# Kernel tuning notes

Measured on AMD Instinct MI355X. Metric: run time of the kernel, lower is better.

Reference implementation:

```python
import jax, jax.numpy as jnp
import numpy as np

NEG_SLOPE = 0.2
EPS = 1e-16

N_NODES = 50000
N_EDGES = 800000
IN_C = 256
HID_C = 64
HEADS = 4
OUT_C = 128
N_GRAPHS = 100


def setup_inputs() -> dict:
    key = jax.random.key(0)
    ks = jax.random.split(key, 12)
    x = jax.random.normal(ks[0], (N_NODES, IN_C), dtype=jnp.float32)
    edge_index = jax.random.randint(ks[1], (2, N_EDGES), 0, N_NODES, dtype=jnp.int64)
    batch = jnp.sort(jax.random.randint(ks[2], (N_NODES,), 0, N_GRAPHS, dtype=jnp.int64))
    s1 = 1.0 / np.sqrt(IN_C)
    s2 = 1.0 / np.sqrt(HEADS * HID_C)
    W1 = jax.random.uniform(ks[3], (IN_C, HEADS * HID_C), jnp.float32, -s1, s1)
    att_src1 = jax.random.uniform(ks[4], (HEADS, HID_C), jnp.float32, -s1, s1)
    att_dst1 = jax.random.uniform(ks[5], (HEADS, HID_C), jnp.float32, -s1, s1)
    bias1 = jnp.zeros((HEADS * HID_C,), jnp.float32)
    W2 = jax.random.uniform(ks[6], (HEADS * HID_C, OUT_C), jnp.float32, -s2, s2)
    att_src2 = jax.random.uniform(ks[7], (1, OUT_C), jnp.float32, -s2, s2)
    att_dst2 = jax.random.uniform(ks[8], (1, OUT_C), jnp.float32, -s2, s2)
    bias2 = jnp.zeros((OUT_C,), jnp.float32)
    return {"x": x, "W1": W1, "att_src1": att_src1, "att_dst1": att_dst1,
            "bias1": bias1, "W2": W2, "att_src2": att_src2, "att_dst2": att_dst2,
            "bias2": bias2, "edge_index": edge_index, "batch": batch,
            "num_graphs": N_GRAPHS}


def gat_conv(x, W, att_src, att_dst, bias, src, dst, heads, ch):
    # x: [N, F_in]; W: [F_in, heads*ch]; att_*: [heads, ch]
    n = x.shape[0]
    h = (x @ W).reshape(n, heads, ch)                      # [N, H, C]
    a_src = jnp.sum(h * att_src[None], axis=-1)            # [N, H]
    a_dst = jnp.sum(h * att_dst[None], axis=-1)            # [N, H]
    alpha = a_src[src] + a_dst[dst]                        # [E, H]
    alpha = jax.nn.leaky_relu(alpha, NEG_SLOPE)
    # segment softmax over destination nodes (every node has a self-loop)
    amax = jax.ops.segment_max(alpha, dst, num_segments=n)
    e = jnp.exp(alpha - amax[dst])
    denom = jax.ops.segment_sum(e, dst, num_segments=n)
    alpha = e / (denom[dst] + EPS)                         # [E, H]
    msg = h[src] * alpha[:, :, None]                       # [E, H, C]
    out = jax.ops.segment_sum(msg, dst, num_segments=n)    # [N, H, C]
    return out.reshape(n, heads * ch) + bias


def reference(x, W1, att_src1, att_dst1, bias1, W2, att_src2, att_dst2, bias2,
              edge_index, batch, num_graphs):
    n = x.shape[0]
    loops = jnp.arange(n, dtype=edge_index.dtype)
    src = jnp.concatenate([edge_index[0], loops])
    dst = jnp.concatenate([edge_index[1], loops])
    h = gat_conv(x, W1, att_src1, att_dst1, bias1, src, dst, HEADS, HID_C)
    h = jax.nn.relu(h)
    h = gat_conv(h, W2, att_src2, att_dst2, bias2, src, dst, 1, OUT_C)
    h = jax.nn.relu(h)
    # global mean pool over graphs
    sums = jax.ops.segment_sum(h, batch, num_segments=num_graphs)
    cnt = jax.ops.segment_sum(jnp.ones((n, 1), h.dtype), batch, num_segments=num_graphs)
    return sums / jnp.maximum(cnt, 1.0)
```

## Files before the change

kernel.cpp:

```cpp
#include <hip/hip_runtime.h>
#include <hip/hip_bf16.h>
#include <hip/hip_fp16.h>

#define N_NODES 50000
#define N_EDGES 800000
#define E_TOT   (N_EDGES + N_NODES)
#define IN_C    256
#define H1C     256
#define HEADS   4
#define HID_C   64
#define OUT_C   128
#define N_GRAPHS 100
#define NEG_SLOPE 0.2f
#define EPS_F 1e-16f

#define NBUCKET 391
#define BIN_BLOCKS 104
#define EDGES_PER_SB 8192
#define EBUF_CAP 4096
#define STAGE_CAP 4096
#define GEMM1_MB 391

#define PREP_CAST_BLOCKS   12500
#define PREP_W1_BLOCKS     256
#define PREP_W2_BLOCKS     128
#define PREP_BOUNDS_BLOCKS 196
#define PREP_ZERO_BLOCKS   52
#define PREP_TOTAL (PREP_CAST_BLOCKS + PREP_W1_BLOCKS + PREP_W2_BLOCKS + PREP_BOUNDS_BLOCKS + PREP_ZERO_BLOCKS)

typedef _Float16 half8_t __attribute__((ext_vector_type(8)));
typedef float f32x4 __attribute__((ext_vector_type(4)));

__global__ __launch_bounds__(256) void prep_kernel(const float* __restrict__ x,
                                                   _Float16* __restrict__ xh,
                                                   const float* __restrict__ W1,
                                                   _Float16* __restrict__ W1t,
                                                   const float* __restrict__ W2,
                                                   _Float16* __restrict__ W2t,
                                                   const int* __restrict__ batch,
                                                   int* __restrict__ gstart,
                                                   int* __restrict__ gcur,
                                                   float* __restrict__ d_out) {
    int b = blockIdx.x;
    int tid = threadIdx.x;
    if (b < PREP_CAST_BLOCKS) {
        int idx = b * 256 + tid;
        float4 v = reinterpret_cast<const float4*>(x)[idx];
        union { _Float16 h[4]; uint2 u; } p;
        p.h[0] = (_Float16)v.x; p.h[1] = (_Float16)v.y;
        p.h[2] = (_Float16)v.z; p.h[3] = (_Float16)v.w;
        reinterpret_cast<uint2*>(xh)[idx] = p.u;
        return;
    }
    b -= PREP_CAST_BLOCKS;
    if (b < PREP_W1_BLOCKS) {
        int idx = b * 256 + tid;
        int n = idx >> 8, k = idx & 255;
        W1t[idx] = (_Float16)W1[k * 256 + n];
        return;
    }
    b -= PREP_W1_BLOCKS;
    if (b < PREP_W2_BLOCKS) {
        int idx = b * 256 + tid;
        int n = idx >> 8, k = idx & 255;
        W2t[idx] = (_Float16)W2[k * 128 + n];
        return;
    }
    b -= PREP_W2_BLOCKS;
    if (b < PREP_BOUNDS_BLOCKS) {
        int idx = b * 256 + tid;
        if (idx >= N_NODES) return;
        int g = batch[idx];
        if (g < 0) g = 0; if (g >= N_GRAPHS) g = N_GRAPHS - 1;
        if (idx == 0) {
            for (int j = 0; j <= g; ++j) gstart[j] = 0;
        } else {
            int gp = batch[idx - 1];
            if (gp < 0) gp = 0; if (gp >= N_GRAPHS) gp = N_GRAPHS - 1;
            for (int j = gp + 1; j <= g; ++j) gstart[j] = idx;
        }
        if (idx == N_NODES - 1) {
            for (int j = g + 1; j <= N_GRAPHS; ++j) gstart[j] = N_NODES;
        }
        return;
    }
    b -= PREP_BOUNDS_BLOCKS;
    {
        int idx = b * 256 + tid;
        if (idx < N_GRAPHS * 128) d_out[idx] = 0.f;
        else {
            int k = idx - N_GRAPHS * 128;
            if (k < 512) gcur[k] = 0;
        }
    }
}

__global__ __launch_bounds__(256) void bucket_bin(const int* __restrict__ ei,
                                                  int* __restrict__ gcur,
                                                  int* __restrict__ ebuf) {
    __shared__ int bh[NBUCKET];
    __shared__ int bofs[NBUCKET];
    int tid = threadIdx.x;
    for (int t = tid; t < NBUCKET; t += 256) bh[t] = 0;
    __syncthreads();
    int base = blockIdx.x * EDGES_PER_SB;
#pragma unroll 4
    for (int k = 0; k < EDGES_PER_SB / 256; ++k) {
        int idx = base + k * 256 + tid;
        int d = -1;
        if (idx < N_EDGES) d = ei[N_EDGES + idx];
        else if (idx < E_TOT) d = idx - N_EDGES;
        if (d >= 0 && d < N_NODES) atomicAdd(&bh[d >> 7], 1);
    }
    __syncthreads();
    for (int t = tid; t < NBUCKET; t += 256) {
        int c = bh[t];
        bofs[t] = (c > 0) ? atomicAdd(&gcur[t], c) : 0;
        bh[t] = 0;
    }
    __syncthreads();
#pragma unroll 4
    for (int k = 0; k < EDGES_PER_SB / 256; ++k) {
        int idx = base + k * 256 + tid;
        int s = 0, d = -1;
        if (idx < N_EDGES) { s = ei[idx]; d = ei[N_EDGES + idx]; }
        else if (idx < E_TOT) { s = idx - N_EDGES; d = s; }
        if (d >= 0 && d < N_NODES) {
            int t = d >> 7;
            int p = bofs[t] + atomicAdd(&bh[t], 1);
            if (p < EBUF_CAP)
                ebuf[t * EBUF_CAP + p] = (s & 0xFFFF) | ((d & 127) << 16);
        }
    }
}

__global__ __launch_bounds__(256) void sort_gemm1_kernel(const int* __restrict__ gcur,
                                                         const int* __restrict__ ebuf,
                                                         int* __restrict__ ssrc,
                                                         int* __restrict__ row_ptr,
                                                         const _Float16* __restrict__ A,
                                                         const _Float16* __restrict__ Bt,
                                                         _Float16* __restrict__ C,
                                                         const float* __restrict__ attS,
                                                         const float* __restrict__ attD,
                                                         float* __restrict__ a_src_o,
                                                         float* __restrict__ a_dst_o) {
    __shared__ __align__(16) char smem[29696];
    __shared__ int s_off;
    const int tid = threadIdx.x;

    if (blockIdx.x < NBUCKET) {
        int* cnt   = reinterpret_cast<int*>(smem);
        int* sc    = cnt + 128;
        int* stage = sc + 128;
        int j = blockIdx.x;
        if (tid < 64) {
            int acc = 0;
            for (int i = tid; i < j; i += 64) {
                int c = gcur[i];
                acc += (c < EBUF_CAP) ? c : EBUF_CAP;
            }
#pragma unroll
            for (int off = 32; off > 0; off >>= 1) acc += __shfl_down(acc, off);
            if (tid == 0) s_off = acc;
        }
        if (tid < 128) cnt[tid] = 0;
        __syncthreads();
        int span = gcur[j]; if (span > EBUF_CAP) span = EBUF_CAP;
        int lo = s_off;
        const int* eb = ebuf + j * EBUF_CAP;
        for (int t = tid; t < span; t += 256)
            atomicAdd(&cnt[(eb[t] >> 16) & 127], 1);
        __syncthreads();
        if (tid < 128) sc[tid] = cnt[tid];
        __syncthreads();
#pragma unroll
        for (int off = 1; off < 128; off <<= 1) {
            int u = (tid >= off && tid < 128) ? sc[tid - off] : 0;
            __syncthreads();
            if (tid < 128) sc[tid] += u;
            __syncthreads();
        }
        int jn0 = j << 7;
        int nNodes = N_NODES - jn0; if (nNodes > 128) nNodes = 128;
        if (tid < 128) {
            int excl = sc[tid] - cnt[tid];
            if (tid < nNodes) row_ptr[jn0 + tid] = lo + excl;
            cnt[tid] = excl;
        }
        if (j == NBUCKET - 1 && tid == 0) row_ptr[N_NODES] = lo + span;
        __syncthreads();
        for (int t = tid; t < span; t += 256) {
            int v = eb[t];
            int p = atomicAdd(&cnt[(v >> 16) & 127], 1);
            stage[p] = v & 0xFFFF;
        }
        __syncthreads();
        for (int t = tid; t < span; t += 256) ssrc[lo + t] = stage[t];
        return;
    }

    _Float16 (*As)[56] = reinterpret_cast<_Float16(*)[56]>(smem);
    _Float16 (*Bs)[56] = reinterpret_cast<_Float16(*)[56]>(smem + 14336);
    float* lds_ps = reinterpret_cast<float*>(smem + 28672);
    float* lds_pd = reinterpret_cast<float*>(smem + 29184);
    (void)lds_ps; (void)lds_pd;
    int b2 = blockIdx.x - NBUCKET;
    const int tileM = (b2 >= GEMM1_MB ? b2 - GEMM1_MB : b2) * 128;
    const int tileN = (b2 >= GEMM1_MB) ? 128 : 0;
    const int w = tid >> 6, lane = tid & 63;
    const int wm = (w >> 1) * 64, wn = (w & 1) * 64;
    const int quad = lane >> 4, mlane = lane & 15;
    const int srow = tid >> 2;
    const int schunk = (tid & 3) * 8;

    f32x4 zero = {0.f, 0.f, 0.f, 0.f};
    f32x4 acc[4][4];
#pragma unroll
    for (int i = 0; i < 4; ++i)
#pragma unroll
        for (int j = 0; j < 4; ++j) acc[i][j] = zero;

    const uint4* Av = reinterpret_cast<const uint4*>(A);
    const uint4* Bv = reinterpret_cast<const uint4*>(Bt);
    const int r0 = tileM + srow, r1 = r0 + 64;
    const bool ok0 = r0 < N_NODES, ok1 = r1 < N_NODES;
    const int bn0 = tileN + srow, bn1 = bn0 + 64;
    const uint4 z4 = make_uint4(0, 0, 0, 0);

    for (int k0 = 0; k0 < 256; k0 += 32) {
        const int kc = (k0 >> 3) + (tid & 3);
        uint4 a0 = ok0 ? Av[(size_t)r0 * 32 + kc] : z4;
        uint4 a1 = ok1 ? Av[(size_t)r1 * 32 + kc] : z4;
        uint4 b0 = Bv[(size_t)bn0 * 32 + kc];
        uint4 b1 = Bv[(size_t)bn1 * 32 + kc];
        __syncthreads();
        *reinterpret_cast<uint4*>(&As[srow][schunk]) = a0;
        *reinterpret_cast<uint4*>(&As[srow + 64][schunk]) = a1;
        *reinterpret_cast<uint4*>(&Bs[srow][schunk]) = b0;
        *reinterpret_cast<uint4*>(&Bs[srow + 64][schunk]) = b1;
        __syncthreads();
        half8_t af[4], bf[4];
#pragma unroll
        for (int mt = 0; mt < 4; ++mt)
            af[mt] = *reinterpret_cast<const half8_t*>(&As[wm + mt * 16 + mlane][quad * 8]);
#pragma unroll
        for (int nt = 0; nt < 4; ++nt)
            bf[nt] = *reinterpret_cast<const half8_t*>(&Bs[wn + nt * 16 + mlane][quad * 8]);
#pragma unroll
        for (int mt = 0; mt < 4; ++mt)
#pragma unroll
            for (int nt = 0; nt < 4; ++nt)
                acc[mt][nt] = __builtin_amdgcn_mfma_f32_16x16x32_f16(af[mt], bf[nt], acc[mt][nt], 0, 0, 0);
    }
#pragma unroll
    for (int mt = 0; mt < 4; ++mt) {
#pragma unroll
        for (int i = 0; i < 4; ++i) {
            int row = tileM + wm + mt * 16 + quad * 4 + i;
            if (row < N_NODES) {
                _Float16* cp = C + (size_t)row * 256 + tileN + wn;
#pragma unroll
                for (int nt = 0; nt < 4; ++nt)
                    cp[nt * 16 + mlane] = (_Float16)acc[mt][nt][i];
            }
        }
    }
    {
        int hd = (tileN + wn) >> 6;
        float as[4], ad[4];
#pragma unroll
        for (int nt = 0; nt < 4; ++nt) {
            as[nt] = attS[hd * 64 + nt * 16 + mlane];
            ad[nt] = attD[hd * 64 + nt * 16 + mlane];
        }
#pragma unroll
        for (int mt = 0; mt < 4; ++mt) {
#pragma unroll
            for (int i = 0; i < 4; ++i) {
                float ps = acc[mt][0][i] * as[0] + acc[mt][1][i] * as[1]
                         + acc[mt][2][i] * as[2] + acc[mt][3][i] * as[3];
                float pd = acc[mt][0][i] * ad[0] + acc[mt][1][i] * ad[1]
                         + acc[mt][2][i] * ad[2] + acc[mt][3][i] * ad[3];
#pragma unroll
                for (int off = 1; off < 16; off <<= 1) {
                    ps += __shfl_xor(ps, off);
                    pd += __shfl_xor(pd, off);
                }
                if (mlane == 0) {
                    int row = tileM + wm + mt * 16 + quad * 4 + i;
                    if (row < N_NODES) {
                        a_src_o[row * 4 + hd] = ps;
                        a_dst_o[row * 4 + hd] = pd;
                    }
                }
            }
        }
    }
}

__global__ __launch_bounds__(256) void gemm_mfma_kernel(const _Float16* __restrict__ A,
                                                        const _Float16* __restrict__ Bt,
                                                        _Float16* __restrict__ C,
                                                        const float* __restrict__ attS,
                                                        const float* __restrict__ attD,
                                                        float* __restrict__ a_src_o,
                                                        float* __restrict__ a_dst_o,
                                                        int M, int N) {
    __shared__ _Float16 As[128][56];
    __shared__ _Float16 Bs[128][56];
    __shared__ float lds_ps[128];
    __shared__ float lds_pd[128];
    const int tid = threadIdx.x;
    const int tileM = blockIdx.x * 128;
    const int tileN = 0;
    const int w = tid >> 6, lane = tid & 63;
    const int wm = (w >> 1) * 64, wn = (w & 1) * 64;
    const int quad = lane >> 4, mlane = lane & 15;
    const int srow = tid >> 2;
    const int schunk = (tid & 3) * 8;

    f32x4 zero = {0.f, 0.f, 0.f, 0.f};
    f32x4 acc[4][4];
#pragma unroll
    for (int i = 0; i < 4; ++i)
#pragma unroll
        for (int j = 0; j < 4; ++j) acc[i][j] = zero;

    const uint4* Av = reinterpret_cast<const uint4*>(A);
    const uint4* Bv = reinterpret_cast<const uint4*>(Bt);
    const int r0 = tileM + srow, r1 = r0 + 64;
    const bool ok0 = r0 < M, ok1 = r1 < M;
    const int bn0 = tileN + srow, bn1 = bn0 + 64;
    const uint4 z4 = make_uint4(0, 0, 0, 0);

    for (int k0 = 0; k0 < 256; k0 += 32) {
        const int kc = (k0 >> 3) + (tid & 3);
        uint4 a0 = ok0 ? Av[(size_t)r0 * 32 + kc] : z4;
        uint4 a1 = ok1 ? Av[(size_t)r1 * 32 + kc] : z4;
        uint4 b0 = Bv[(size_t)bn0 * 32 + kc];
        uint4 b1 = Bv[(size_t)bn1 * 32 + kc];
        __syncthreads();
        *reinterpret_cast<uint4*>(&As[srow][schunk]) = a0;
        *reinterpret_cast<uint4*>(&As[srow + 64][schunk]) = a1;
        *reinterpret_cast<uint4*>(&Bs[srow][schunk]) = b0;
        *reinterpret_cast<uint4*>(&Bs[srow + 64][schunk]) = b1;
        __syncthreads();
        half8_t af[4], bf[4];
#pragma unroll
        for (int mt = 0; mt < 4; ++mt)
            af[mt] = *reinterpret_cast<const half8_t*>(&As[wm + mt * 16 + mlane][quad * 8]);
#pragma unroll
        for (int nt = 0; nt < 4; ++nt)
            bf[nt] = *reinterpret_cast<const half8_t*>(&Bs[wn + nt * 16 + mlane][quad * 8]);
#pragma unroll
        for (int mt = 0; mt < 4; ++mt)
#pragma unroll
            for (int nt = 0; nt < 4; ++nt)
                acc[mt][nt] = __builtin_amdgcn_mfma_f32_16x16x32_f16(af[mt], bf[nt], acc[mt][nt], 0, 0, 0);
    }
#pragma unroll
    for (int mt = 0; mt < 4; ++mt) {
#pragma unroll
        for (int i = 0; i < 4; ++i) {
            int row = tileM + wm + mt * 16 + quad * 4 + i;
            if (row < M) {
                _Float16* cp = C + (size_t)row * N + tileN + wn;
#pragma unroll
                for (int nt = 0; nt < 4; ++nt)
                    cp[nt * 16 + mlane] = (_Float16)acc[mt][nt][i];
            }
        }
    }
    {
        float as[4], ad[4];
#pragma unroll
        for (int nt = 0; nt < 4; ++nt) {
            as[nt] = attS[wn + nt * 16 + mlane];
            ad[nt] = attD[wn + nt * 16 + mlane];
        }
        float psa[4][4], pda[4][4];
#pragma unroll
        for (int mt = 0; mt < 4; ++mt) {
#pragma unroll
            for (int i = 0; i < 4; ++i) {
                float ps = acc[mt][0][i] * as[0] + acc[mt][1][i] * as[1]
                         + acc[mt][2][i] * as[2] + acc[mt][3][i] * as[3];
                float pd = acc[mt][0][i] * ad[0] + acc[mt][1][i] * ad[1]
                         + acc[mt][2][i] * ad[2] + acc[mt][3][i] * ad[3];
#pragma unroll
                for (int off = 1; off < 16; off <<= 1) {
                    ps += __shfl_xor(ps, off);
                    pd += __shfl_xor(pd, off);
                }
                psa[mt][i] = ps; pda[mt][i] = pd;
            }
        }
        __syncthreads();
        if (wn == 0 && mlane == 0) {
#pragma unroll
            for (int mt = 0; mt < 4; ++mt)
#pragma unroll
                for (int i = 0; i < 4; ++i) {
                    int lr = wm + mt * 16 + quad * 4 + i;
                    lds_ps[lr] = psa[mt][i];
                    lds_pd[lr] = pda[mt][i];
                }
        }
        __syncthreads();
        if (wn == 64 && mlane == 0) {
#pragma unroll
            for (int mt = 0; mt < 4; ++mt)
#pragma unroll
                for (int i = 0; i < 4; ++i) {
                    int lr = wm + mt * 16 + quad * 4 + i;
                    int row = tileM + lr;
                    if (row < M) {
                        a_src_o[row] = psa[mt][i] + lds_ps[lr];
                        a_dst_o[row] = pda[mt][i] + lds_pd[lr];
                    }
                }
        }
    }
}

__device__ __forceinline__ float lrelu(float x) { return x > 0.f ? x : NEG_SLOPE * x; }

__global__ __launch_bounds__(256) void edge1_kernel(const int* __restrict__ row_ptr,
                                                    const int* __restrict__ ssrc,
                                                    const __half* __restrict__ h1h,
                                                    const float* __restrict__ a_src,
                                                    const float* __restrict__ a_dst,
                                                    const float* __restrict__ bias,
                                                    __half* __restrict__ out) {
    int node = blockIdx.x * 4 + (threadIdx.x >> 6);
    int lane = threadIdx.x & 63;
    int hf   = lane >> 5;
    int cl   = lane & 31;
    int hd   = cl >> 3;
    int start = row_ptr[node], end = row_ptr[node + 1];
    int em1 = end - 1;
    float adh = a_dst[node * 4 + hd];

    const uint4* h1v = reinterpret_cast<const uint4*>(h1h);
    float4 aA0 = make_float4(0.f,0.f,0.f,0.f), aA1 = make_float4(0.f,0.f,0.f,0.f);
    float4 aB0 = make_float4(0.f,0.f,0.f,0.f), aB1 = make_float4(0.f,0.f,0.f,0.f);
    float s = 0.f;
    for (int e = start; e < end; e += 4) {
        int e0 = e + hf;
        int e1 = e + 2 + hf;
        int i0 = ssrc[e0 <= em1 ? e0 : em1];
        int i1 = ssrc[e1 <= em1 ? e1 : em1];
        float r0 = a_src[i0 * 4 + hd];
        float r1 = a_src[i1 * 4 + hd];
        uint4 q0 = h1v[(size_t)i0 * 32 + cl];
        uint4 q1 = h1v[(size_t)i1 * 32 + cl];
        float w0 = (e0 < end) ? __expf(lrelu(r0 + adh)) : 0.f;
        float w1 = (e1 < end) ? __expf(lrelu(r1 + adh)) : 0.f;
        s += w0 + w1;
        float2 f;
        f = __half22float2(*reinterpret_cast<const __half2*>(&q0.x)); aA0.x += w0*f.x; aA0.y += w0*f.y;
        f = __half22float2(*reinterpret_cast<const __half2*>(&q0.y)); aA0.z += w0*f.x; aA0.w += w0*f.y;
        f = __half22float2(*reinterpret_cast<const __half2*>(&q0.z)); aA1.x += w0*f.x; aA1.y += w0*f.y;
        f = __half22float2(*reinterpret_cast<const __half2*>(&q0.w)); aA1.z += w0*f.x; aA1.w += w0*f.y;
        f = __half22float2(*reinterpret_cast<const __half2*>(&q1.x)); aB0.x += w1*f.x; aB0.y += w1*f.y;
        f = __half22float2(*reinterpret_cast<const __half2*>(&q1.y)); aB0.z += w1*f.x; aB0.w += w1*f.y;
        f = __half22float2(*reinterpret_cast<const __half2*>(&q1.z)); aB1.x += w1*f.x; aB1.y += w1*f.y;
        f = __half22float2(*reinterpret_cast<const __half2*>(&q1.w)); aB1.z += w1*f.x; aB1.w += w1*f.y;
    }
    float4 c0, c1;
    c0.x = aA0.x + aB0.x; c0.y = aA0.y + aB0.y; c0.z = aA0.z + aB0.z; c0.w = aA0.w + aB0.w;
    c1.x = aA1.x + aB1.x; c1.y = aA1.y + aB1.y; c1.z = aA1.z + aB1.z; c1.w = aA1.w + aB1.w;
    c0.x += __shfl_xor(c0.x, 32); c0.y += __shfl_xor(c0.y, 32);
    c0.z += __shfl_xor(c0.z, 32); c0.w += __shfl_xor(c0.w, 32);
    c1.x += __shfl_xor(c1.x, 32); c1.y += __shfl_xor(c1.y, 32);
    c1.z += __shfl_xor(c1.z, 32); c1.w += __shfl_xor(c1.w, 32);
    s += __shfl_xor(s, 32);
    float inv = 1.0f / (s + EPS_F);
    if (lane < 32) {
        const float4* b4 = reinterpret_cast<const float4*>(bias);
        float4 b0 = b4[cl * 2], b1 = b4[cl * 2 + 1];
        union { _Float16 h[8]; uint4 u; } st;
        st.h[0] = (_Float16)fmaxf(c0.x * inv + b0.x, 0.f);
        st.h[1] = (_Float16)fmaxf(c0.y * inv + b0.y, 0.f);
        st.h[2] = (_Float16)fmaxf(c0.z * inv + b0.z, 0.f);
        st.h[3] = (_Float16)fmaxf(c0.w * inv + b0.w, 0.f);
        st.h[4] = (_Float16)fmaxf(c1.x * inv + b1.x, 0.f);
        st.h[5] = (_Float16)fmaxf(c1.y * inv + b1.y, 0.f);
        st.h[6] = (_Float16)fmaxf(c1.z * inv + b1.z, 0.f);
        st.h[7] = (_Float16)fmaxf(c1.w * inv + b1.w, 0.f);
        reinterpret_cast<uint4*>(out)[(size_t)node * 32 + cl] = st.u;
    }
}

__global__ __launch_bounds__(256) void edge2_kernel(const int* __restrict__ row_ptr,
                                                    const int* __restrict__ ssrc,
                                                    const __half* __restrict__ h2h,
                                                    const float* __restrict__ a_src,
                                                    const float* __restrict__ a_dst,
                                                    const float* __restrict__ bias,
                                                    float* __restrict__ out) {
    int lane = threadIdx.x & 63;
    int node = blockIdx.x * 8 + ((threadIdx.x >> 6) << 1) + (lane >> 5);
    int sub  = (lane >> 4) & 1;
    int cl   = lane & 15;
    int start = row_ptr[node], end = row_ptr[node + 1];
    int em1 = end - 1;
    float ad = a_dst[node];

    const uint4* h2v = reinterpret_cast<const uint4*>(h2h);
    float4 aA0 = make_float4(0.f,0.f,0.f,0.f), aA1 = make_float4(0.f,0.f,0.f,0.f);
    float4 aB0 = make_float4(0.f,0.f,0.f,0.f), aB1 = make_float4(0.f,0.f,0.f,0.f);
    float s = 0.f;
    for (int e = start; e < end; e += 4) {
        int e0 = e + sub;
        int e1 = e + 2 + sub;
        int i0 = ssrc[e0 <= em1 ? e0 : em1];
        int i1 = ssrc[e1 <= em1 ? e1 : em1];
        float r0 = a_src[i0];
        float r1 = a_src[i1];
        uint4 q0 = h2v[(size_t)i0 * 16 + cl];
        uint4 q1 = h2v[(size_t)i1 * 16 + cl];
        float w0 = (e0 < end) ? __expf(lrelu(r0 + ad)) : 0.f;
        float w1 = (e1 < end) ? __expf(lrelu(r1 + ad)) : 0.f;
        s += w0 + w1;
        float2 f;
        f = __half22float2(*reinterpret_cast<const __half2*>(&q0.x)); aA0.x += w0*f.x; aA0.y += w0*f.y;
        f = __half22float2(*reinterpret_cast<const __half2*>(&q0.y)); aA0.z += w0*f.x; aA0.w += w0*f.y;
        f = __half22float2(*reinterpret_cast<const __half2*>(&q0.z)); aA1.x += w0*f.x; aA1.y += w0*f.y;
        f = __half22float2(*reinterpret_cast<const __half2*>(&q0.w)); aA1.z += w0*f.x; aA1.w += w0*f.y;
        f = __half22float2(*reinterpret_cast<const __half2*>(&q1.x)); aB0.x += w1*f.x; aB0.y += w1*f.y;
        f = __half22float2(*reinterpret_cast<const __half2*>(&q1.y)); aB0.z += w1*f.x; aB0.w += w1*f.y;
        f = __half22float2(*reinterpret_cast<const __half2*>(&q1.z)); aB1.x += w1*f.x; aB1.y += w1*f.y;
        f = __half22float2(*reinterpret_cast<const __half2*>(&q1.w)); aB1.z += w1*f.x; aB1.w += w1*f.y;
    }
    float4 c0, c1;
    c0.x = aA0.x + aB0.x; c0.y = aA0.y + aB0.y; c0.z = aA0.z + aB0.z; c0.w = aA0.w + aB0.w;
    c1.x = aA1.x + aB1.x; c1.y = aA1.y + aB1.y; c1.z = aA1.z + aB1.z; c1.w = aA1.w + aB1.w;
    c0.x += __shfl_xor(c0.x, 16); c0.y += __shfl_xor(c0.y, 16);
    c0.z += __shfl_xor(c0.z, 16); c0.w += __shfl_xor(c0.w, 16);
    c1.x += __shfl_xor(c1.x, 16); c1.y += __shfl_xor(c1.y, 16);
    c1.z += __shfl_xor(c1.z, 16); c1.w += __shfl_xor(c1.w, 16);
    s += __shfl_xor(s, 16);
    float inv = 1.0f / (s + EPS_F);
    if (sub == 0) {
        const float4* b4 = reinterpret_cast<const float4*>(bias);
        float4 b0 = b4[cl * 2], b1 = b4[cl * 2 + 1];
        float4 o0, o1;
        o0.x = fmaxf(c0.x * inv + b0.x, 0.f);
        o0.y = fmaxf(c0.y * inv + b0.y, 0.f);
        o0.z = fmaxf(c0.z * inv + b0.z, 0.f);
        o0.w = fmaxf(c0.w * inv + b0.w, 0.f);
        o1.x = fmaxf(c1.x * inv + b1.x, 0.f);
        o1.y = fmaxf(c1.y * inv + b1.y, 0.f);
        o1.z = fmaxf(c1.z * inv + b1.z, 0.f);
        o1.w = fmaxf(c1.w * inv + b1.w, 0.f);
        float4* o4 = reinterpret_cast<float4*>(out) + (size_t)node * 32 + cl * 2;
        o4[0] = o0;
        o4[1] = o1;
    }
}

#define POOL_CHUNK 64
__global__ __launch_bounds__(128) void pool_kernel(const float* __restrict__ out2,
                                                   const int* __restrict__ batch,
                                                   const int* __restrict__ gstart,
                                                   float* __restrict__ d_out) {
    int c = threadIdx.x;
    int node0 = blockIdx.x * POOL_CHUNK;
    int nodeEnd = node0 + POOL_CHUNK; if (nodeEnd > N_NODES) nodeEnd = N_NODES;
    if (node0 >= N_NODES) return;
    int gprev = batch[node0];
    float acc = 0.f;
    for (int node = node0; node < nodeEnd; ++node) {
        int g = batch[node];
        if (g != gprev) {
            if (gprev >= 0 && gprev < N_GRAPHS) {
                float cnt = (float)(gstart[gprev + 1] - gstart[gprev]);
                if (cnt < 1.f) cnt = 1.f;
                atomicAdd(&d_out[gprev * 128 + c], acc / cnt);
            }
            acc = 0.f;
            gprev = g;
        }
        acc += out2[(size_t)node * 128 + c];
    }
    if (gprev >= 0 && gprev < N_GRAPHS) {
        float cnt = (float)(gstart[gprev + 1] - gstart[gprev]);
        if (cnt < 1.f) cnt = 1.f;
        atomicAdd(&d_out[gprev * 128 + c], acc / cnt);
    }
}

extern "C" void kernel_launch(void* const* d_in, const int* in_sizes, int n_in,
                              void* d_out_v, int out_size, void* d_ws, size_t ws_size,
                              hipStream_t stream) {
    const float* x      = (const float*)d_in[0];
    const float* W1     = (const float*)d_in[1];
    const float* att_s1 = (const float*)d_in[2];
    const float* att_d1 = (const float*)d_in[3];
    const float* bias1  = (const float*)d_in[4];
    const float* W2     = (const float*)d_in[5];
    const float* att_s2 = (const float*)d_in[6];
    const float* att_d2 = (const float*)d_in[7];
    const float* bias2  = (const float*)d_in[8];
    const int*   ei     = (const int*)d_in[9];
    const int*   batch  = (const int*)d_in[10];
    float* d_out = (float*)d_out_v;

    float* ws = (float*)d_ws;
    _Float16* xh    = (_Float16*)ws;
    _Float16* h1h   = (_Float16*)(ws + 6400000);
    _Float16* out1h = (_Float16*)(ws + 12800000);
    _Float16* h2h   = (_Float16*)ws;
    float*    out2  = ws + 6400000;
    float* a_src1 = ws + 19200000;
    float* a_dst1 = a_src1 + 200000;
    float* a_src2 = a_dst1 + 200000;
    float* a_dst2 = a_src2 + 50000;
    int* row_ptr  = (int*)(a_dst2 + 50000);
    int* ssrc     = row_ptr + 50016;
    int* ebuf     = ssrc + 850000;
    int* gcur     = ebuf + (NBUCKET * EBUF_CAP);
    int* gstart   = gcur + 512;
    _Float16* W1t = (_Float16*)(gstart + 128);
    _Float16* W2t = W1t + 65536;

    prep_kernel<<<PREP_TOTAL, 256, 0, stream>>>(x, xh, W1, W1t, W2, W2t,
                                                batch, gstart, gcur, d_out);

    bucket_bin<<<BIN_BLOCKS, 256, 0, stream>>>(ei, gcur, ebuf);

    sort_gemm1_kernel<<<NBUCKET + GEMM1_MB * 2, 256, 0, stream>>>(
        gcur, ebuf, ssrc, row_ptr, xh, W1t, h1h,
        att_s1, att_d1, a_src1, a_dst1);

    edge1_kernel<<<N_NODES / 4, 256, 0, stream>>>(row_ptr, ssrc, (const __half*)h1h,
                                                  a_src1, a_dst1, bias1, (__half*)out1h);

    gemm_mfma_kernel<<<(N_NODES + 127) / 128, 256, 0, stream>>>(
        out1h, W2t, h2h, att_s2, att_d2, a_src2, a_dst2, N_NODES, OUT_C);

    edge2_kernel<<<N_NODES / 8, 256, 0, stream>>>(row_ptr, ssrc, (const __half*)h2h,
                                                  a_src2, a_dst2, bias2, out2);

    pool_kernel<<<(N_NODES + POOL_CHUNK - 1) / POOL_CHUNK, 128, 0, stream>>>(out2, batch, gstart, d_out);
}
```

Before: 299.6 us.

## Fuse edge binning into prep kernel and use direct global-to-LDS swizzled GEMM loads

Folds the separate bucket_bin kernel into extra blocks of prep_kernel, with a hipMemsetAsync clearing gcur beforehand, so the edge binning overlaps the casts and one kernel launch is removed. Both MFMA GEMM kernels now stage A/B tiles with global_load_lds 16-byte loads straight into a compact XOR-swizzled LDS layout. This avoids the register round-trip and the padded shared arrays, and shrinks LDS use. The row bounds checks on A are dropped, so the last tile reads past the valid rows into the workspace; those rows are never stored. An extra memset operation is added to the stream.

```diff
diff --git a/kernel.cpp b/kernel.cpp
--- a/kernel.cpp
+++ b/kernel.cpp
@@ -21,15 +21,22 @@
 #define STAGE_CAP 4096
 #define GEMM1_MB 391
 
+#define PREP_BIN_BLOCKS    104
 #define PREP_CAST_BLOCKS   12500
 #define PREP_W1_BLOCKS     256
 #define PREP_W2_BLOCKS     128
 #define PREP_BOUNDS_BLOCKS 196
-#define PREP_ZERO_BLOCKS   52
-#define PREP_TOTAL (PREP_CAST_BLOCKS + PREP_W1_BLOCKS + PREP_W2_BLOCKS + PREP_BOUNDS_BLOCKS + PREP_ZERO_BLOCKS)
+#define PREP_DOUT_BLOCKS   50
+#define PREP_TOTAL (PREP_BIN_BLOCKS + PREP_CAST_BLOCKS + PREP_W1_BLOCKS + PREP_W2_BLOCKS + PREP_BOUNDS_BLOCKS + PREP_DOUT_BLOCKS)
 
 typedef _Float16 half8_t __attribute__((ext_vector_type(8)));
 typedef float f32x4 __attribute__((ext_vector_type(4)));
+
+__device__ __forceinline__ void gll16(const void* g, void* l) {
+    __builtin_amdgcn_global_load_lds(
+        (const __attribute__((address_space(1))) void*)g,
+        (__attribute__((address_space(3))) void*)l, 16, 0, 0);
+}
 
 __global__ __launch_bounds__(256) void prep_kernel(const float* __restrict__ x,
                                                    _Float16* __restrict__ xh,
@@ -37,12 +44,51 @@
                                                    _Float16* __restrict__ W1t,
                                                    const float* __restrict__ W2,
                                                    _Float16* __restrict__ W2t,
+                                                   const int* __restrict__ ei,
+                                                   int* __restrict__ gcur,
+                                                   int* __restrict__ ebuf,
                                                    const int* __restrict__ batch,
                                                    int* __restrict__ gstart,
-                                                   int* __restrict__ gcur,
                                                    float* __restrict__ d_out) {
+    __shared__ int bh[NBUCKET];
+    __shared__ int bofs[NBUCKET];
     int b = blockIdx.x;
     int tid = threadIdx.x;
+    if (b < PREP_BIN_BLOCKS) {
+        for (int t = tid; t < NBUCKET; t += 256) bh[t] = 0;
+        __syncthreads();
+        int base = b * EDGES_PER_SB;
+#pragma unroll 4
+        for (int k = 0; k < EDGES_PER_SB / 256; ++k) {
+            int idx = base + k * 256 + tid;
+            int d = -1;
+            if (idx < N_EDGES) d = ei[N_EDGES + idx];
+            else if (idx < E_TOT) d = idx - N_EDGES;
+            if (d >= 0 && d < N_NODES) atomicAdd(&bh[d >> 7], 1);
+        }
+        __syncthreads();
+        for (int t = tid; t < NBUCKET; t += 256) {
+            int c = bh[t];
+            bofs[t] = (c > 0) ? atomicAdd(&gcur[t], c) : 0;
+            bh[t] = 0;
+        }
+        __syncthreads();
+#pragma unroll 4
+        for (int k = 0; k < EDGES_PER_SB / 256; ++k) {
+            int idx = base + k * 256 + tid;
+            int s = 0, d = -1;
+            if (idx < N_EDGES) { s = ei[idx]; d = ei[N_EDGES + idx]; }
+            else if (idx < E_TOT) { s = idx - N_EDGES; d = s; }
+            if (d >= 0 && d < N_NODES) {
+                int t = d >> 7;
+                int p = bofs[t] + atomicAdd(&bh[t], 1);
+                if (p < EBUF_CAP)
+                    ebuf[t * EBUF_CAP + p] = (s & 0xFFFF) | ((d & 127) << 16);
+            }
+        }
+        return;
+    }
+    b -= PREP_BIN_BLOCKS;
     if (b < PREP_CAST_BLOCKS) {
         int idx = b * 256 + tid;
         float4 v = reinterpret_cast<const float4*>(x)[idx];
@@ -88,49 +134,6 @@
     {
         int idx = b * 256 + tid;
         if (idx < N_GRAPHS * 128) d_out[idx] = 0.f;
-        else {
-            int k = idx - N_GRAPHS * 128;
-            if (k < 512) gcur[k] = 0;
-        }
-    }
-}
-
-__global__ __launch_bounds__(256) void bucket_bin(const int* __restrict__ ei,
-                                                  int* __restrict__ gcur,
-                                                  int* __restrict__ ebuf) {
-    __shared__ int bh[NBUCKET];
-    __shared__ int bofs[NBUCKET];
-    int tid = threadIdx.x;
-    for (int t = tid; t < NBUCKET; t += 256) bh[t] = 0;
-    __syncthreads();
-    int base = blockIdx.x * EDGES_PER_SB;
-#pragma unroll 4
-    for (int k = 0; k < EDGES_PER_SB / 256; ++k) {
-        int idx = base + k * 256 + tid;
-        int d = -1;
-        if (idx < N_EDGES) d = ei[N_EDGES + idx];
-        else if (idx < E_TOT) d = idx - N_EDGES;
-        if (d >= 0 && d < N_NODES) atomicAdd(&bh[d >> 7], 1);
-    }
-    __syncthreads();
-    for (int t = tid; t < NBUCKET; t += 256) {
-        int c = bh[t];
-        bofs[t] = (c > 0) ? atomicAdd(&gcur[t], c) : 0;
-        bh[t] = 0;
-    }
-    __syncthreads();
-#pragma unroll 4
-    for (int k = 0; k < EDGES_PER_SB / 256; ++k) {
-        int idx = base + k * 256 + tid;
-        int s = 0, d = -1;
-        if (idx < N_EDGES) { s = ei[idx]; d = ei[N_EDGES + idx]; }
-        else if (idx < E_TOT) { s = idx - N_EDGES; d = s; }
-        if (d >= 0 && d < N_NODES) {
-            int t = d >> 7;
-            int p = bofs[t] + atomicAdd(&bh[t], 1);
-            if (p < EBUF_CAP)
-                ebuf[t * EBUF_CAP + p] = (s & 0xFFFF) | ((d & 127) << 16);
-        }
     }
 }
 
@@ -145,7 +148,7 @@
                                                          const float* __restrict__ attD,
                                                          float* __restrict__ a_src_o,
                                                          float* __restrict__ a_dst_o) {
-    __shared__ __align__(16) char smem[29696];
+    __shared__ __align__(16) char smem[17408];
     __shared__ int s_off;
     const int tid = threadIdx.x;
 
@@ -200,19 +203,20 @@
         return;
     }
 
-    _Float16 (*As)[56] = reinterpret_cast<_Float16(*)[56]>(smem);
-    _Float16 (*Bs)[56] = reinterpret_cast<_Float16(*)[56]>(smem + 14336);
-    float* lds_ps = reinterpret_cast<float*>(smem + 28672);
-    float* lds_pd = reinterpret_cast<float*>(smem + 29184);
-    (void)lds_ps; (void)lds_pd;
+    _Float16* As = reinterpret_cast<_Float16*>(smem);
+    _Float16* Bs = reinterpret_cast<_Float16*>(smem + 8192);
     int b2 = blockIdx.x - NBUCKET;
     const int tileM = (b2 >= GEMM1_MB ? b2 - GEMM1_MB : b2) * 128;
     const int tileN = (b2 >= GEMM1_MB) ? 128 : 0;
     const int w = tid >> 6, lane = tid & 63;
     const int wm = (w >> 1) * 64, wn = (w & 1) * 64;
     const int quad = lane >> 4, mlane = lane & 15;
-    const int srow = tid >> 2;
-    const int schunk = (tid & 3) * 8;
+    const int lrow = lane >> 2;
+    const int pos  = lane & 3;
+    const int ra0  = w * 16 + lrow;
+    const int ra1  = ra0 + 64;
+    const int ca0  = pos ^ ((ra0 >> 1) & 3);
+    const int ca1  = pos ^ ((ra1 >> 1) & 3);
 
     f32x4 zero = {0.f, 0.f, 0.f, 0.f};
     f32x4 acc[4][4];
@@ -221,32 +225,33 @@
 #pragma unroll
         for (int j = 0; j < 4; ++j) acc[i][j] = zero;
 
-    const uint4* Av = reinterpret_cast<const uint4*>(A);
-    const uint4* Bv = reinterpret_cast<const uint4*>(Bt);
-    const int r0 = tileM + srow, r1 = r0 + 64;
-    const bool ok0 = r0 < N_NODES, ok1 = r1 < N_NODES;
-    const int bn0 = tileN + srow, bn1 = bn0 + 64;
-    const uint4 z4 = make_uint4(0, 0, 0, 0);
+    const _Float16* gA0 = A + (size_t)(tileM + ra0) * 256 + ca0 * 8;
+    const _Float16* gA1 = A + (size_t)(tileM + ra1) * 256 + ca1 * 8;
+    const _Float16* gB0 = Bt + (size_t)(tileN + ra0) * 256 + ca0 * 8;
+    const _Float16* gB1 = Bt + (size_t)(tileN + ra1) * 256 + ca1 * 8;
+    _Float16* lA0 = As + w * 512;
+    _Float16* lA1 = As + 2048 + w * 512;
+    _Float16* lB0 = Bs + w * 512;
+    _Float16* lB1 = Bs + 2048 + w * 512;
 
     for (int k0 = 0; k0 < 256; k0 += 32) {
-        const int kc = (k0 >> 3) + (tid & 3);
-        uint4 a0 = ok0 ? Av[(size_t)r0 * 32 + kc] : z4;
-        uint4 a1 = ok1 ? Av[(size_t)r1 * 32 + kc] : z4;
-        uint4 b0 = Bv[(size_t)bn0 * 32 + kc];
-        uint4 b1 = Bv[(size_t)bn1 * 32 + kc];
-        __syncthreads();
-        *reinterpret_cast<uint4*>(&As[srow][schunk]) = a0;
-        *reinterpret_cast<uint4*>(&As[srow + 64][schunk]) = a1;
-        *reinterpret_cast<uint4*>(&Bs[srow][schunk]) = b0;
-        *reinterpret_cast<uint4*>(&Bs[srow + 64][schunk]) = b1;
+        __syncthreads();
+        gll16(gA0 + k0, lA0);
+        gll16(gA1 + k0, lA1);
+        gll16(gB0 + k0, lB0);
+        gll16(gB1 + k0, lB1);
         __syncthreads();
         half8_t af[4], bf[4];
 #pragma unroll
-        for (int mt = 0; mt < 4; ++mt)
-            af[mt] = *reinterpret_cast<const half8_t*>(&As[wm + mt * 16 + mlane][quad * 8]);
-#pragma unroll
-        for (int nt = 0; nt < 4; ++nt)
-            bf[nt] = *reinterpret_cast<const half8_t*>(&Bs[wn + nt * 16 + mlane][quad * 8]);
+        for (int mt = 0; mt < 4; ++mt) {
+            int ra = wm + mt * 16 + mlane;
+            af[mt] = *reinterpret_cast<const half8_t*>(As + ra * 32 + ((quad ^ ((ra >> 1) & 3)) << 3));
+        }
+#pragma unroll
+        for (int nt = 0; nt < 4; ++nt) {
+            int rb = wn + nt * 16 + mlane;
+            bf[nt] = *reinterpret_cast<const half8_t*>(Bs + rb * 32 + ((quad ^ ((rb >> 1) & 3)) << 3));
+        }
 #pragma unroll
         for (int mt = 0; mt < 4; ++mt)
 #pragma unroll
@@ -307,8 +312,8 @@
                                                         float* __restrict__ a_src_o,
                                                         float* __restrict__ a_dst_o,
                                                         int M, int N) {
-    __shared__ _Float16 As[128][56];
-    __shared__ _Float16 Bs[128][56];
+    __shared__ __align__(16) _Float16 As[4096];
+    __shared__ __align__(16) _Float16 Bs[4096];
     __shared__ float lds_ps[128];
     __shared__ float lds_pd[128];
     const int tid = threadIdx.x;
@@ -317,8 +322,12 @@
     const int w = tid >> 6, lane = tid & 63;
     const int wm = (w >> 1) * 64, wn = (w & 1) * 64;
     const int quad = lane >> 4, mlane = lane & 15;
-    const int srow = tid >> 2;
-    const int schunk = (tid & 3) * 8;
+    const int lrow = lane >> 2;
+    const int pos  = lane & 3;
+    const int ra0  = w * 16 + lrow;
+    const int ra1  = ra0 + 64;
+    const int ca0  = pos ^ ((ra0 >> 1) & 3);
+    const int ca1  = pos ^ ((ra1 >> 1) & 3);
 
     f32x4 zero = {0.f, 0.f, 0.f, 0.f};
     f32x4 acc[4][4];
@@ -327,32 +336,33 @@
 #pragma unroll
         for (int j = 0; j < 4; ++j) acc[i][j] = zero;
 
-    const uint4* Av = reinterpret_cast<const uint4*>(A);
-    const uint4* Bv = reinterpret_cast<const uint4*>(Bt);
-    const int r0 = tileM + srow, r1 = r0 + 64;
-    const bool ok0 = r0 < M, ok1 = r1 < M;
-    const int bn0 = tileN + srow, bn1 = bn0 + 64;
-    const uint4 z4 = make_uint4(0, 0, 0, 0);
+    const _Float16* gA0 = A + (size_t)(tileM + ra0) * 256 + ca0 * 8;
+    const _Float16* gA1 = A + (size_t)(tileM + ra1) * 256 + ca1 * 8;
+    const _Float16* gB0 = Bt + (size_t)(tileN + ra0) * 256 + ca0 * 8;
+    const _Float16* gB1 = Bt + (size_t)(tileN + ra1) * 256 + ca1 * 8;
+    _Float16* lA0 = As + w * 512;
+    _Float16* lA1 = As + 2048 + w * 512;
+    _Float16* lB0 = Bs + w * 512;
+    _Float16* lB1 = Bs + 2048 + w * 512;
 
     for (int k0 = 0; k0 < 256; k0 += 32) {
-        const int kc = (k0 >> 3) + (tid & 3);
-        uint4 a0 = ok0 ? Av[(size_t)r0 * 32 + kc] : z4;
-        uint4 a1 = ok1 ? Av[(size_t)r1 * 32 + kc] : z4;
-        uint4 b0 = Bv[(size_t)bn0 * 32 + kc];
-        uint4 b1 = Bv[(size_t)bn1 * 32 + kc];
-        __syncthreads();
-        *reinterpret_cast<uint4*>(&As[srow][schunk]) = a0;
-        *reinterpret_cast<uint4*>(&As[srow + 64][schunk]) = a1;
-        *reinterpret_cast<uint4*>(&Bs[srow][schunk]) = b0;
-        *reinterpret_cast<uint4*>(&Bs[srow + 64][schunk]) = b1;
+        __syncthreads();
+        gll16(gA0 + k0, lA0);
+        gll16(gA1 + k0, lA1);
+        gll16(gB0 + k0, lB0);
+        gll16(gB1 + k0, lB1);
         __syncthreads();
         half8_t af[4], bf[4];
 #pragma unroll
-        for (int mt = 0; mt < 4; ++mt)
-            af[mt] = *reinterpret_cast<const half8_t*>(&As[wm + mt * 16 + mlane][quad * 8]);
-#pragma unroll
-        for (int nt = 0; nt < 4; ++nt)
-            bf[nt] = *reinterpret_cast<const half8_t*>(&Bs[wn + nt * 16 + mlane][quad * 8]);
+        for (int mt = 0; mt < 4; ++mt) {
+            int ra = wm + mt * 16 + mlane;
+            af[mt] = *reinterpret_cast<const half8_t*>(As + ra * 32 + ((quad ^ ((ra >> 1) & 3)) << 3));
+        }
+#pragma unroll
+        for (int nt = 0; nt < 4; ++nt) {
+            int rb = wn + nt * 16 + mlane;
+            bf[nt] = *reinterpret_cast<const half8_t*>(Bs + rb * 32 + ((quad ^ ((rb >> 1) & 3)) << 3));
+        }
 #pragma unroll
         for (int mt = 0; mt < 4; ++mt)
 #pragma unroll
@@ -626,10 +636,11 @@
     _Float16* W1t = (_Float16*)(gstart + 128);
     _Float16* W2t = W1t + 65536;
 
+    hipMemsetAsync(gcur, 0, 512 * sizeof(int), stream);
+
     prep_kernel<<<PREP_TOTAL, 256, 0, stream>>>(x, xh, W1, W1t, W2, W2t,
-                                                batch, gstart, gcur, d_out);
-
-    bucket_bin<<<BIN_BLOCKS, 256, 0, stream>>>(ei, gcur, ebuf);
+                                                ei, gcur, ebuf,
+                                                batch, gstart, d_out);
 
     sort_gemm1_kernel<<<NBUCKET + GEMM1_MB * 2, 256, 0, stream>>>(
         gcur, ebuf, ssrc, row_ptr, xh, W1t, h1h,
```

After: 293.3 us. 1.02x faster.
